# Performance work log

Measured on AMD Instinct MI355X. Metric: run time of the kernel, lower is better.

The kernel has to match this reference:

```python
import jax, jax.numpy as jnp
from jax import lax
import numpy as np

BETA = 0.9   # snn.Leaky(beta=0.9)
THR = 1.0    # snntorch default threshold, reset_mechanism='subtract'

@jax.custom_vjp
def spike(x):
    return (x > 0.0).astype(x.dtype)

def _spike_fwd(x):
    return spike(x), x

def _spike_bwd(x, g):
    # snntorch surrogate.atan (alpha=2): dS/dx = 1 / (1 + (pi*x)^2)
    return (g / (1.0 + (jnp.pi * x) ** 2),)

spike.defvjp(_spike_fwd, _spike_bwd)

def lif(inp, mem):
    # snntorch Leaky: reset based on PREVIOUS mem, detached; subtract mechanism
    reset = lax.stop_gradient(spike(mem - THR))
    mem = BETA * mem + inp - reset * THR
    return spike(mem - THR), mem

def conv1d(x, w, b):
    # x: (B, Cin, L), w: (Cout, Cin, K), VALID padding
    y = lax.conv_general_dilated(x, w, window_strides=(1,), padding='VALID',
                                 dimension_numbers=('NCH', 'OIH', 'NCH'))
    return y + b[None, :, None]

def setup_inputs() -> dict:
    key = jax.random.key(0)
    ks = jax.random.split(key, 11)
    B, L, T, num_c = 1024, 30, 100, 10
    def init(k, shape, fan_in):
        bound = 1.0 / np.sqrt(fan_in)
        return jax.random.uniform(k, shape, jnp.float32, -bound, bound)
    return {
        'x':   jax.random.normal(ks[0], (B, 1, L, T), jnp.float32),
        'w1':  init(ks[1], (16, 1, 7), 1 * 7),   'b1': init(ks[2], (16,), 7),
        'w2':  init(ks[3], (32, 16, 5), 16 * 5), 'b2': init(ks[4], (32,), 80),
        'w3':  init(ks[5], (64, 32, 3), 32 * 3), 'b3': init(ks[6], (64,), 96),
        'fw1': init(ks[7], (256, 64 * 18), 64 * 18), 'fb1': init(ks[8], (256,), 64 * 18),
        'fw2': init(ks[9], (num_c, 256), 256),       'fb2': init(ks[10], (num_c,), 256),
    }

def reference(x, w1, b1, w2, b2, w3, b3, fw1, fb1, fw2, fb2):
    B = x.shape[0]
    num_c = fw2.shape[0]
    xt_seq = jnp.transpose(x, (3, 0, 1, 2))  # (T, B, 1, 30)
    mems = (jnp.zeros((B, 16, 24), x.dtype),  # after conv1 (k=7): 30->24
            jnp.zeros((B, 32, 20), x.dtype),  # after conv2 (k=5): 24->20
            jnp.zeros((B, 64, 18), x.dtype),  # after conv3 (k=3): 20->18
            jnp.zeros((B, 256), x.dtype),
            jnp.zeros((B, num_c), x.dtype))
    def step(mems, xt):
        m1, m2, m3, m4, m5 = mems
        h = conv1d(xt, w1, b1); s, m1 = lif(h, m1)
        h = conv1d(s, w2, b2);  s, m2 = lif(h, m2)
        h = conv1d(s, w3, b3);  s, m3 = lif(h, m3)
        h = s.reshape(B, -1) @ fw1.T + fb1; s, m4 = lif(h, m4)
        h = s @ fw2.T + fb2;               s, m5 = lif(h, m5)
        return (m1, m2, m3, m4, m5), s
    _, spk_rec = lax.scan(step, mems, xt_seq)
    return spk_rec  # (T, B, num_c) -- matches torch.stack(spk_rec)
```

## Files before the change

kernel.cpp:

```cpp
#include <hip/hip_runtime.h>
#include <stdint.h>

#define BETA 0.9f

__global__ void transpose_fw1(const float* __restrict__ A, float* __restrict__ At) {
    __shared__ float tile[32][33];
    const int i0 = blockIdx.x * 32;
    const int j0 = blockIdx.y * 32;
    const int tx = threadIdx.x, ty = threadIdx.y;
    for (int r = ty; r < 32; r += 8)
        tile[r][tx] = A[(j0 + r) * 1152 + i0 + tx];
    __syncthreads();
    for (int r = ty; r < 32; r += 8)
        At[(i0 + r) * 256 + j0 + tx] = tile[tx][r];
}

__global__ __launch_bounds__(768)
__attribute__((amdgpu_waves_per_eu(6)))
void snn_main(
    const float* __restrict__ x,
    const float* __restrict__ w1, const float* __restrict__ b1,
    const float* __restrict__ w2, const float* __restrict__ b2,
    const float* __restrict__ w3, const float* __restrict__ b3,
    const float* __restrict__ fw1T,
    const float* __restrict__ fb1,
    const float* __restrict__ fw2, const float* __restrict__ fb2,
    float* __restrict__ out)
{
    const int b    = blockIdx.x;
    const int tid  = threadIdx.x;
    const int e    = (tid >= 384) ? 1 : 0;
    const int tl   = tid - 384 * e;
    const int lane = tid & 63;
    const int ew   = tl >> 6;

    __shared__ float w2L[16 * 5 * 32];
    __shared__ float w3L[32 * 3 * 64];
    __shared__ float pacc[2][6][256];
    __shared__ float s1e[2][16 * 24 + 8];
    __shared__ float s4[2][256];
    __shared__ unsigned long long masks[2][2][18];
    __shared__ unsigned int rm1[2][2][16];
    __shared__ unsigned int cm2[2][2][20];

    const int c1 = tl & 15;
    const int l1 = tl >> 4;
    const int c2 = tl & 31;
    const int g2 = tl >> 5;
    const int l02 = 2 * g2;
    const bool c2on = (ew < 5);
    const unsigned wmask2 = 0x3Fu << l02;
    const int c3 = lane;
    const int l03 = ew * 3;
    const int rl = tl - 320;

    for (int i = tid; i < 16 * 5 * 32; i += 768) {
        const int cc = i & 31, r = i >> 5;
        w2L[i] = w2[cc * 80 + r];
    }
    for (int i = tid; i < 32 * 3 * 64; i += 768) {
        const int cc = i & 63, r = i >> 6;
        w3L[i] = w3[cc * 96 + r];
    }
    if (tl < 16) { rm1[e][0][tl] = 0u; rm1[e][1][tl] = 0u; }
    if (tl < 20) { cm2[e][0][tl] = 0u; cm2[e][1][tl] = 0u; }
    if (tl < 8)  s1e[e][384 + tl] = 0.0f;

    float w1r[7];
#pragma unroll
    for (int k = 0; k < 7; ++k) w1r[k] = w1[c1 * 7 + k];
    const float b1r = b1[c1];
    const float b2r = b2[c2];
    const float b3r = b3[c3];
    const int jf = tl >> 4, chf = tl & 15;
    const float fb2r = (tl < 160 && chf == 0) ? fb2[jf] : 0.0f;
    float fb1q[4];
#pragma unroll
    for (int q = 0; q < 4; ++q)
        fb1q[q] = (ew == 5) ? fb1[rl + 64 * q] : 0.0f;

    float m1 = 0.f;
    float m2[2] = {0.f, 0.f};
    float m3[3] = {0.f, 0.f, 0.f};
    float m4q[4] = {0.f, 0.f, 0.f, 0.f};
    float m5 = 0.f;

    const float* xb = x + (2 * b + e) * 3000;
    const int out_b = (2 * b + e) * 10;
    const float4* fw1Tv = reinterpret_cast<const float4*>(fw1T);

    float xr[7];
#pragma unroll
    for (int k = 0; k < 7; ++k) xr[k] = xb[(l1 + k) * 100];

    __syncthreads();

    {
        float h = b1r;
#pragma unroll
        for (int k = 0; k < 7; ++k) h += xr[k] * w1r[k];
        float rs = (m1 > 1.0f) ? 1.0f : 0.0f;
        m1 = BETA * m1 + h - rs;
        float sa = (m1 > 1.0f) ? 1.0f : 0.0f;
        s1e[e][c1 * 24 + l1] = sa;
        if (sa != 0.0f) atomicOr(&rm1[e][0][c1], 1u << l1);
    }
    __syncthreads();

    for (int tau = 0; tau < 102; ++tau) {
        const int pb = tau & 1, pn = pb ^ 1;

        if (tl < 16) rm1[e][pn][tl] = 0u;
        if (tl < 20) cm2[e][pn][tl] = 0u;
        if (tau <= 98) {
#pragma unroll
            for (int k = 0; k < 7; ++k) xr[k] = xb[(l1 + k) * 100 + tau + 1];
        }
        if (c2on) {
            if (tau <= 99) {
                float h[2] = {b2r, b2r};
#pragma unroll
                for (int ci = 0; ci < 16; ++ci) {
                    const unsigned rmv =
                        __builtin_amdgcn_readfirstlane(rm1[e][pb][ci]);
                    if ((rmv & wmask2) == 0u) continue;
                    float win[6];
#pragma unroll
                    for (int r = 0; r < 6; ++r) win[r] = s1e[e][ci * 24 + l02 + r];
                    float wk[5];
#pragma unroll
                    for (int k = 0; k < 5; ++k) wk[k] = w2L[(ci * 5 + k) * 32 + c2];
#pragma unroll
                    for (int li = 0; li < 2; ++li)
#pragma unroll
                        for (int k = 0; k < 5; ++k) h[li] += win[li + k] * wk[k];
                }
#pragma unroll
                for (int li = 0; li < 2; ++li) {
                    float rs = (m2[li] > 1.0f) ? 1.0f : 0.0f;
                    m2[li] = BETA * m2[li] + h[li] - rs;
                    if (m2[li] > 1.0f) atomicOr(&cm2[e][pb][l02 + li], 1u << c2);
                }
            }
        } else {
            if (tau >= 2) {
#pragma unroll
                for (int q = 0; q < 4; ++q) {
                    const int j = rl + 64 * q;
                    float acc = fb1q[q];
#pragma unroll
                    for (int w = 0; w < 6; ++w) acc += pacc[e][w][j];
                    float rs = (m4q[q] > 1.0f) ? 1.0f : 0.0f;
                    m4q[q] = BETA * m4q[q] + acc - rs;
                    s4[e][j] = (m4q[q] > 1.0f) ? 1.0f : 0.0f;
                }
            }
        }
        __syncthreads();

        if (tau <= 98) {
            float h = b1r;
#pragma unroll
            for (int k = 0; k < 7; ++k) h += xr[k] * w1r[k];
            float rs = (m1 > 1.0f) ? 1.0f : 0.0f;
            m1 = BETA * m1 + h - rs;
            float sa = (m1 > 1.0f) ? 1.0f : 0.0f;
            s1e[e][c1 * 24 + l1] = sa;
            if (sa != 0.0f) atomicOr(&rm1[e][pn][c1], 1u << l1);
        }

        if (tau <= 99) {
            float h[3] = {b3r, b3r, b3r};
#pragma unroll
            for (int wl = 0; wl < 5; ++wl) {
                unsigned cm = __builtin_amdgcn_readfirstlane(cm2[e][pb][l03 + wl]);
                while (cm) {
                    const int ci = (int)__builtin_ctz(cm); cm &= cm - 1;
                    const float* wp = &w3L[ci * 192 + c3];
#pragma unroll
                    for (int k = 0; k < 3; ++k) {
                        const int li = wl - k;
                        if (li >= 0 && li < 3)
                            h[li] += wp[k * 64];
                    }
                }
            }
#pragma unroll
            for (int li = 0; li < 3; ++li) {
                float rs = (m3[li] > 1.0f) ? 1.0f : 0.0f;
                m3[li] = BETA * m3[li] + h[li] - rs;
                float s = (m3[li] > 1.0f) ? 1.0f : 0.0f;
                unsigned long long mk = __ballot(s != 0.0f);
                if (lane == 0) masks[e][pb][l03 + li] = mk;
            }
        }

        if (tau >= 1 && tau <= 100) {
            float4 acc4; acc4.x = acc4.y = acc4.z = acc4.w = 0.0f;
#pragma unroll 1
            for (int l = ew; l < 18; l += 6) {
                const unsigned* mp = (const unsigned*)&masks[e][pn][l];
                const unsigned mlo = __builtin_amdgcn_readfirstlane(mp[0]);
                const unsigned mhi = __builtin_amdgcn_readfirstlane(mp[1]);
                unsigned long long mk = ((unsigned long long)mhi << 32) | mlo;
                while (mk) {
                    float4 f0, f1, f2, f3;
                    f0.x=f0.y=f0.z=f0.w=0.f; f1=f0; f2=f0; f3=f0;
                    int c;
                    c = (int)__builtin_ctzll(mk); mk &= mk - 1;
                    f0 = fw1Tv[(c * 18 + l) * 64 + lane];
                    if (mk) { c = (int)__builtin_ctzll(mk); mk &= mk - 1;
                              f1 = fw1Tv[(c * 18 + l) * 64 + lane]; }
                    if (mk) { c = (int)__builtin_ctzll(mk); mk &= mk - 1;
                              f2 = fw1Tv[(c * 18 + l) * 64 + lane]; }
                    if (mk) { c = (int)__builtin_ctzll(mk); mk &= mk - 1;
                              f3 = fw1Tv[(c * 18 + l) * 64 + lane]; }
                    acc4.x += f0.x; acc4.y += f0.y; acc4.z += f0.z; acc4.w += f0.w;
                    acc4.x += f1.x; acc4.y += f1.y; acc4.z += f1.z; acc4.w += f1.w;
                    acc4.x += f2.x; acc4.y += f2.y; acc4.z += f2.z; acc4.w += f2.w;
                    acc4.x += f3.x; acc4.y += f3.y; acc4.z += f3.z; acc4.w += f3.w;
                }
            }
            ((float4*)&pacc[e][ew][0])[lane] = acc4;
        }

        if (tau >= 2 && tl < 160) {
            const int t5 = tau - 2;
            const float* wrow = fw2 + jf * 256;
            float p = 0.f;
#pragma unroll
            for (int i = 0; i < 16; ++i)
                p += s4[e][i * 16 + chf] * wrow[i * 16 + chf];
            p += __shfl_xor(p, 8, 16);
            p += __shfl_xor(p, 4, 16);
            p += __shfl_xor(p, 2, 16);
            p += __shfl_xor(p, 1, 16);
            if (chf == 0) {
                float h = fb2r + p;
                float rs = (m5 > 1.0f) ? 1.0f : 0.0f;
                m5 = BETA * m5 + h - rs;
                out[t5 * 10240 + out_b + jf] = (m5 > 1.0f) ? 1.0f : 0.0f;
            }
        }
        __syncthreads();
    }
}

extern "C" void kernel_launch(void* const* d_in, const int* in_sizes, int n_in,
                              void* d_out, int out_size, void* d_ws, size_t ws_size,
                              hipStream_t stream) {
    const float* x   = (const float*)d_in[0];
    const float* w1  = (const float*)d_in[1];
    const float* b1  = (const float*)d_in[2];
    const float* w2  = (const float*)d_in[3];
    const float* b2  = (const float*)d_in[4];
    const float* w3  = (const float*)d_in[5];
    const float* b3  = (const float*)d_in[6];
    const float* fw1 = (const float*)d_in[7];
    const float* fb1 = (const float*)d_in[8];
    const float* fw2 = (const float*)d_in[9];
    const float* fb2 = (const float*)d_in[10];
    float* out  = (float*)d_out;
    float* fw1T = (float*)d_ws;

    dim3 tb(32, 8);
    dim3 tg(1152 / 32, 256 / 32);
    transpose_fw1<<<tg, tb, 0, stream>>>(fw1, fw1T);
    snn_main<<<512, 768, 0, stream>>>(x, w1, b1, w2, b2, w3, b3,
                                      fw1T, fb1, fw2, fb2, out);
}
```

Baseline: 679.5 us.

## Restage SNN pipeline to cut one step of latency and use bitmask conv2

Reorders the per-timestep phases so conv3 and the output layer run in one barrier interval and conv1 plus fc1 run in the next. This shortens the pipeline from 102 to 101 iterations and lets the masks buffer be single-buffered. Conv2 now reads spike bits directly from the bitmask and does conditional adds instead of multiply-adds over a shared spike array, so s1e is removed. The w3 shared layout is changed to [ci][c][k], which adds strided-by-3 LDS access per lane and so risks bank conflicts.

After: 677.9 us. Within noise of the previous version (-0.2%).

```diff
diff --git a/kernel.cpp b/kernel.cpp
--- a/kernel.cpp
+++ b/kernel.cpp
@@ -35,11 +35,10 @@
     const int ew   = tl >> 6;
 
     __shared__ float w2L[16 * 5 * 32];
-    __shared__ float w3L[32 * 3 * 64];
+    __shared__ float w3L[32 * 64 * 3];
     __shared__ float pacc[2][6][256];
-    __shared__ float s1e[2][16 * 24 + 8];
     __shared__ float s4[2][256];
-    __shared__ unsigned long long masks[2][2][18];
+    __shared__ unsigned long long masks[2][18];
     __shared__ unsigned int rm1[2][2][16];
     __shared__ unsigned int cm2[2][2][20];
 
@@ -48,8 +47,7 @@
     const int c2 = tl & 31;
     const int g2 = tl >> 5;
     const int l02 = 2 * g2;
-    const bool c2on = (ew < 5);
-    const unsigned wmask2 = 0x3Fu << l02;
+    const bool c2w = (ew < 5);
     const int c3 = lane;
     const int l03 = ew * 3;
     const int rl = tl - 320;
@@ -58,13 +56,13 @@
         const int cc = i & 31, r = i >> 5;
         w2L[i] = w2[cc * 80 + r];
     }
-    for (int i = tid; i < 32 * 3 * 64; i += 768) {
-        const int cc = i & 63, r = i >> 6;
-        w3L[i] = w3[cc * 96 + r];
+    for (int i = tid; i < 32 * 64 * 3; i += 768) {
+        const int ci = i / 192, r2 = i - ci * 192;
+        const int cc = r2 / 3, k = r2 - cc * 3;
+        w3L[i] = w3[cc * 96 + ci * 3 + k];
     }
     if (tl < 16) { rm1[e][0][tl] = 0u; rm1[e][1][tl] = 0u; }
     if (tl < 20) { cm2[e][0][tl] = 0u; cm2[e][1][tl] = 0u; }
-    if (tl < 8)  s1e[e][384 + tl] = 0.0f;
 
     float w1r[7];
 #pragma unroll
@@ -101,13 +99,11 @@
         for (int k = 0; k < 7; ++k) h += xr[k] * w1r[k];
         float rs = (m1 > 1.0f) ? 1.0f : 0.0f;
         m1 = BETA * m1 + h - rs;
-        float sa = (m1 > 1.0f) ? 1.0f : 0.0f;
-        s1e[e][c1 * 24 + l1] = sa;
-        if (sa != 0.0f) atomicOr(&rm1[e][0][c1], 1u << l1);
+        if (m1 > 1.0f) atomicOr(&rm1[e][0][c1], 1u << l1);
     }
     __syncthreads();
 
-    for (int tau = 0; tau < 102; ++tau) {
+    for (int tau = 0; tau <= 100; ++tau) {
         const int pb = tau & 1, pn = pb ^ 1;
 
         if (tl < 16) rm1[e][pn][tl] = 0u;
@@ -116,58 +112,48 @@
 #pragma unroll
             for (int k = 0; k < 7; ++k) xr[k] = xb[(l1 + k) * 100 + tau + 1];
         }
-        if (c2on) {
+        if (c2w) {
             if (tau <= 99) {
-                float h[2] = {b2r, b2r};
+                float h0 = b2r, h1 = b2r;
 #pragma unroll
                 for (int ci = 0; ci < 16; ++ci) {
                     const unsigned rmv =
                         __builtin_amdgcn_readfirstlane(rm1[e][pb][ci]);
-                    if ((rmv & wmask2) == 0u) continue;
-                    float win[6];
-#pragma unroll
-                    for (int r = 0; r < 6; ++r) win[r] = s1e[e][ci * 24 + l02 + r];
+                    const unsigned wb = (rmv >> l02) & 0x3Fu;
+                    if (wb == 0u) continue;
                     float wk[5];
 #pragma unroll
-                    for (int k = 0; k < 5; ++k) wk[k] = w2L[(ci * 5 + k) * 32 + c2];
-#pragma unroll
-                    for (int li = 0; li < 2; ++li)
-#pragma unroll
-                        for (int k = 0; k < 5; ++k) h[li] += win[li + k] * wk[k];
-                }
-#pragma unroll
-                for (int li = 0; li < 2; ++li) {
-                    float rs = (m2[li] > 1.0f) ? 1.0f : 0.0f;
-                    m2[li] = BETA * m2[li] + h[li] - rs;
-                    if (m2[li] > 1.0f) atomicOr(&cm2[e][pb][l02 + li], 1u << c2);
-                }
-            }
-        } else {
-            if (tau >= 2) {
-#pragma unroll
-                for (int q = 0; q < 4; ++q) {
-                    const int j = rl + 64 * q;
-                    float acc = fb1q[q];
-#pragma unroll
-                    for (int w = 0; w < 6; ++w) acc += pacc[e][w][j];
-                    float rs = (m4q[q] > 1.0f) ? 1.0f : 0.0f;
-                    m4q[q] = BETA * m4q[q] + acc - rs;
-                    s4[e][j] = (m4q[q] > 1.0f) ? 1.0f : 0.0f;
-                }
+                    for (int k = 0; k < 5; ++k)
+                        wk[k] = w2L[(ci * 5 + k) * 32 + c2];
+                    if (wb & 1u)  h0 += wk[0];
+                    if (wb & 2u)  { h0 += wk[1]; h1 += wk[0]; }
+                    if (wb & 4u)  { h0 += wk[2]; h1 += wk[1]; }
+                    if (wb & 8u)  { h0 += wk[3]; h1 += wk[2]; }
+                    if (wb & 16u) { h0 += wk[4]; h1 += wk[3]; }
+                    if (wb & 32u) h1 += wk[4];
+                }
+                {
+                    float rs = (m2[0] > 1.0f) ? 1.0f : 0.0f;
+                    m2[0] = BETA * m2[0] + h0 - rs;
+                    if (m2[0] > 1.0f) atomicOr(&cm2[e][pb][l02], 1u << c2);
+                    rs = (m2[1] > 1.0f) ? 1.0f : 0.0f;
+                    m2[1] = BETA * m2[1] + h1 - rs;
+                    if (m2[1] > 1.0f) atomicOr(&cm2[e][pb][l02 + 1], 1u << c2);
+                }
+            }
+        } else if (tau >= 1) {
+#pragma unroll
+            for (int q = 0; q < 4; ++q) {
+                const int j = rl + 64 * q;
+                float acc = fb1q[q];
+#pragma unroll
+                for (int w = 0; w < 6; ++w) acc += pacc[e][w][j];
+                float rs = (m4q[q] > 1.0f) ? 1.0f : 0.0f;
+                m4q[q] = BETA * m4q[q] + acc - rs;
+                s4[e][j] = (m4q[q] > 1.0f) ? 1.0f : 0.0f;
             }
         }
         __syncthreads();
-
-        if (tau <= 98) {
-            float h = b1r;
-#pragma unroll
-            for (int k = 0; k < 7; ++k) h += xr[k] * w1r[k];
-            float rs = (m1 > 1.0f) ? 1.0f : 0.0f;
-            m1 = BETA * m1 + h - rs;
-            float sa = (m1 > 1.0f) ? 1.0f : 0.0f;
-            s1e[e][c1 * 24 + l1] = sa;
-            if (sa != 0.0f) atomicOr(&rm1[e][pn][c1], 1u << l1);
-        }
 
         if (tau <= 99) {
             float h[3] = {b3r, b3r, b3r};
@@ -176,12 +162,12 @@
                 unsigned cm = __builtin_amdgcn_readfirstlane(cm2[e][pb][l03 + wl]);
                 while (cm) {
                     const int ci = (int)__builtin_ctz(cm); cm &= cm - 1;
-                    const float* wp = &w3L[ci * 192 + c3];
+                    const float* wp = &w3L[ci * 192 + c3 * 3];
 #pragma unroll
                     for (int k = 0; k < 3; ++k) {
                         const int li = wl - k;
                         if (li >= 0 && li < 3)
-                            h[li] += wp[k * 64];
+                            h[li] += wp[k];
                     }
                 }
             }
@@ -191,15 +177,43 @@
                 m3[li] = BETA * m3[li] + h[li] - rs;
                 float s = (m3[li] > 1.0f) ? 1.0f : 0.0f;
                 unsigned long long mk = __ballot(s != 0.0f);
-                if (lane == 0) masks[e][pb][l03 + li] = mk;
-            }
-        }
-
-        if (tau >= 1 && tau <= 100) {
+                if (lane == 0) masks[e][l03 + li] = mk;
+            }
+        }
+        if (tau >= 1 && tl < 160) {
+            const int t5 = tau - 1;
+            const float* wrow = fw2 + jf * 256;
+            float p = 0.f;
+#pragma unroll
+            for (int i = 0; i < 16; ++i)
+                p += s4[e][i * 16 + chf] * wrow[i * 16 + chf];
+            p += __shfl_xor(p, 8, 16);
+            p += __shfl_xor(p, 4, 16);
+            p += __shfl_xor(p, 2, 16);
+            p += __shfl_xor(p, 1, 16);
+            if (chf == 0) {
+                float h = fb2r + p;
+                float rs = (m5 > 1.0f) ? 1.0f : 0.0f;
+                m5 = BETA * m5 + h - rs;
+                out[t5 * 10240 + out_b + jf] = (m5 > 1.0f) ? 1.0f : 0.0f;
+            }
+        }
+        __syncthreads();
+
+        if (tau <= 98) {
+            float h = b1r;
+#pragma unroll
+            for (int k = 0; k < 7; ++k) h += xr[k] * w1r[k];
+            float rs = (m1 > 1.0f) ? 1.0f : 0.0f;
+            m1 = BETA * m1 + h - rs;
+            if (m1 > 1.0f) atomicOr(&rm1[e][pn][c1], 1u << l1);
+        }
+
+        if (tau <= 99) {
             float4 acc4; acc4.x = acc4.y = acc4.z = acc4.w = 0.0f;
 #pragma unroll 1
             for (int l = ew; l < 18; l += 6) {
-                const unsigned* mp = (const unsigned*)&masks[e][pn][l];
+                const unsigned* mp = (const unsigned*)&masks[e][l];
                 const unsigned mlo = __builtin_amdgcn_readfirstlane(mp[0]);
                 const unsigned mhi = __builtin_amdgcn_readfirstlane(mp[1]);
                 unsigned long long mk = ((unsigned long long)mhi << 32) | mlo;
@@ -223,25 +237,6 @@
             }
             ((float4*)&pacc[e][ew][0])[lane] = acc4;
         }
-
-        if (tau >= 2 && tl < 160) {
-            const int t5 = tau - 2;
-            const float* wrow = fw2 + jf * 256;
-            float p = 0.f;
-#pragma unroll
-            for (int i = 0; i < 16; ++i)
-                p += s4[e][i * 16 + chf] * wrow[i * 16 + chf];
-            p += __shfl_xor(p, 8, 16);
-            p += __shfl_xor(p, 4, 16);
-            p += __shfl_xor(p, 2, 16);
-            p += __shfl_xor(p, 1, 16);
-            if (chf == 0) {
-                float h = fb2r + p;
-                float rs = (m5 > 1.0f) ? 1.0f : 0.0f;
-                m5 = BETA * m5 + h - rs;
-                out[t5 * 10240 + out_b + jf] = (m5 > 1.0f) ? 1.0f : 0.0f;
-            }
-        }
         __syncthreads();
     }
 }
```

## Restructure timestep pipeline: fuse FC2 into FC1 wave, add barrier phase

Applied to the files above, without the earlier changes.

Moves the layer-5 (fc2 + LIF) computation into the sixth wave, right after the fc1 LIF update, so s4 is consumed in the same phase it is produced. Conv3 gets its own barrier-separated phase, which removes one stage of pipeline delay: the loop runs 101 iterations instead of 102 and the masks buffer is no longer double-buffered. The cost is a third __syncthreads per timestep and fc2 work serialized onto a single wave, with each lane group handling up to three outputs.

Measured after the change: 779.6 us. 1.15x slower.

```diff
diff --git a/kernel.cpp b/kernel.cpp
--- a/kernel.cpp
+++ b/kernel.cpp
@@ -39,7 +39,7 @@
     __shared__ float pacc[2][6][256];
     __shared__ float s1e[2][16 * 24 + 8];
     __shared__ float s4[2][256];
-    __shared__ unsigned long long masks[2][2][18];
+    __shared__ unsigned long long masks[2][18];
     __shared__ unsigned int rm1[2][2][16];
     __shared__ unsigned int cm2[2][2][20];
 
@@ -48,11 +48,11 @@
     const int c2 = tl & 31;
     const int g2 = tl >> 5;
     const int l02 = 2 * g2;
-    const bool c2on = (ew < 5);
+    const bool c2w = (ew < 5);
     const unsigned wmask2 = 0x3Fu << l02;
     const int c3 = lane;
     const int l03 = ew * 3;
-    const int rl = tl - 320;
+    const int g5 = lane >> 4, chf5 = lane & 15;
 
     for (int i = tid; i < 16 * 5 * 32; i += 768) {
         const int cc = i & 31, r = i >> 5;
@@ -72,18 +72,21 @@
     const float b1r = b1[c1];
     const float b2r = b2[c2];
     const float b3r = b3[c3];
-    const int jf = tl >> 4, chf = tl & 15;
-    const float fb2r = (tl < 160 && chf == 0) ? fb2[jf] : 0.0f;
-    float fb1q[4];
+    float fb1q[4], fb2q[3];
 #pragma unroll
     for (int q = 0; q < 4; ++q)
-        fb1q[q] = (ew == 5) ? fb1[rl + 64 * q] : 0.0f;
+        fb1q[q] = (ew == 5) ? fb1[lane + 64 * q] : 0.0f;
+#pragma unroll
+    for (int pi = 0; pi < 3; ++pi) {
+        const int jj = g5 + 4 * pi;
+        fb2q[pi] = (ew == 5 && chf5 == 0 && jj < 10) ? fb2[jj] : 0.0f;
+    }
 
     float m1 = 0.f;
     float m2[2] = {0.f, 0.f};
     float m3[3] = {0.f, 0.f, 0.f};
     float m4q[4] = {0.f, 0.f, 0.f, 0.f};
-    float m5 = 0.f;
+    float m5q[3] = {0.f, 0.f, 0.f};
 
     const float* xb = x + (2 * b + e) * 3000;
     const int out_b = (2 * b + e) * 10;
@@ -107,7 +110,7 @@
     }
     __syncthreads();
 
-    for (int tau = 0; tau < 102; ++tau) {
+    for (int tau = 0; tau <= 100; ++tau) {
         const int pb = tau & 1, pn = pb ^ 1;
 
         if (tl < 16) rm1[e][pn][tl] = 0u;
@@ -116,7 +119,7 @@
 #pragma unroll
             for (int k = 0; k < 7; ++k) xr[k] = xb[(l1 + k) * 100 + tau + 1];
         }
-        if (c2on) {
+        if (c2w) {
             if (tau <= 99) {
                 float h[2] = {b2r, b2r};
 #pragma unroll
@@ -142,18 +145,66 @@
                     if (m2[li] > 1.0f) atomicOr(&cm2[e][pb][l02 + li], 1u << c2);
                 }
             }
-        } else {
-            if (tau >= 2) {
-#pragma unroll
-                for (int q = 0; q < 4; ++q) {
-                    const int j = rl + 64 * q;
-                    float acc = fb1q[q];
-#pragma unroll
-                    for (int w = 0; w < 6; ++w) acc += pacc[e][w][j];
-                    float rs = (m4q[q] > 1.0f) ? 1.0f : 0.0f;
-                    m4q[q] = BETA * m4q[q] + acc - rs;
-                    s4[e][j] = (m4q[q] > 1.0f) ? 1.0f : 0.0f;
-                }
+        } else if (tau >= 1) {
+            const int t45 = tau - 1;
+#pragma unroll
+            for (int q = 0; q < 4; ++q) {
+                const int j = lane + 64 * q;
+                float acc = fb1q[q];
+#pragma unroll
+                for (int w = 0; w < 6; ++w) acc += pacc[e][w][j];
+                float rs = (m4q[q] > 1.0f) ? 1.0f : 0.0f;
+                m4q[q] = BETA * m4q[q] + acc - rs;
+                s4[e][j] = (m4q[q] > 1.0f) ? 1.0f : 0.0f;
+            }
+#pragma unroll
+            for (int pi = 0; pi < 3; ++pi) {
+                const int jj = g5 + 4 * pi;
+                if (jj < 10) {
+                    const float* wrow = fw2 + jj * 256;
+                    float p = 0.f;
+#pragma unroll
+                    for (int i = 0; i < 16; ++i)
+                        p += s4[e][i * 16 + chf5] * wrow[i * 16 + chf5];
+                    p += __shfl_xor(p, 8, 16);
+                    p += __shfl_xor(p, 4, 16);
+                    p += __shfl_xor(p, 2, 16);
+                    p += __shfl_xor(p, 1, 16);
+                    if (chf5 == 0) {
+                        float h = fb2q[pi] + p;
+                        float rs = (m5q[pi] > 1.0f) ? 1.0f : 0.0f;
+                        m5q[pi] = BETA * m5q[pi] + h - rs;
+                        out[t45 * 10240 + out_b + jj] =
+                            (m5q[pi] > 1.0f) ? 1.0f : 0.0f;
+                    }
+                }
+            }
+        }
+        __syncthreads();
+
+        if (tau <= 99) {
+            float h[3] = {b3r, b3r, b3r};
+#pragma unroll
+            for (int wl = 0; wl < 5; ++wl) {
+                unsigned cm = __builtin_amdgcn_readfirstlane(cm2[e][pb][l03 + wl]);
+                while (cm) {
+                    const int ci = (int)__builtin_ctz(cm); cm &= cm - 1;
+                    const float* wp = &w3L[ci * 192 + c3];
+#pragma unroll
+                    for (int k = 0; k < 3; ++k) {
+                        const int li = wl - k;
+                        if (li >= 0 && li < 3)
+                            h[li] += wp[k * 64];
+                    }
+                }
+            }
+#pragma unroll
+            for (int li = 0; li < 3; ++li) {
+                float rs = (m3[li] > 1.0f) ? 1.0f : 0.0f;
+                m3[li] = BETA * m3[li] + h[li] - rs;
+                float s = (m3[li] > 1.0f) ? 1.0f : 0.0f;
+                unsigned long long mk = __ballot(s != 0.0f);
+                if (lane == 0) masks[e][l03 + li] = mk;
             }
         }
         __syncthreads();
@@ -170,36 +221,10 @@
         }
 
         if (tau <= 99) {
-            float h[3] = {b3r, b3r, b3r};
-#pragma unroll
-            for (int wl = 0; wl < 5; ++wl) {
-                unsigned cm = __builtin_amdgcn_readfirstlane(cm2[e][pb][l03 + wl]);
-                while (cm) {
-                    const int ci = (int)__builtin_ctz(cm); cm &= cm - 1;
-                    const float* wp = &w3L[ci * 192 + c3];
-#pragma unroll
-                    for (int k = 0; k < 3; ++k) {
-                        const int li = wl - k;
-                        if (li >= 0 && li < 3)
-                            h[li] += wp[k * 64];
-                    }
-                }
-            }
-#pragma unroll
-            for (int li = 0; li < 3; ++li) {
-                float rs = (m3[li] > 1.0f) ? 1.0f : 0.0f;
-                m3[li] = BETA * m3[li] + h[li] - rs;
-                float s = (m3[li] > 1.0f) ? 1.0f : 0.0f;
-                unsigned long long mk = __ballot(s != 0.0f);
-                if (lane == 0) masks[e][pb][l03 + li] = mk;
-            }
-        }
-
-        if (tau >= 1 && tau <= 100) {
             float4 acc4; acc4.x = acc4.y = acc4.z = acc4.w = 0.0f;
 #pragma unroll 1
             for (int l = ew; l < 18; l += 6) {
-                const unsigned* mp = (const unsigned*)&masks[e][pn][l];
+                const unsigned* mp = (const unsigned*)&masks[e][l];
                 const unsigned mlo = __builtin_amdgcn_readfirstlane(mp[0]);
                 const unsigned mhi = __builtin_amdgcn_readfirstlane(mp[1]);
                 unsigned long long mk = ((unsigned long long)mhi << 32) | mlo;
@@ -223,25 +248,6 @@
             }
             ((float4*)&pacc[e][ew][0])[lane] = acc4;
         }
-
-        if (tau >= 2 && tl < 160) {
-            const int t5 = tau - 2;
-            const float* wrow = fw2 + jf * 256;
-            float p = 0.f;
-#pragma unroll
-            for (int i = 0; i < 16; ++i)
-                p += s4[e][i * 16 + chf] * wrow[i * 16 + chf];
-            p += __shfl_xor(p, 8, 16);
-            p += __shfl_xor(p, 4, 16);
-            p += __shfl_xor(p, 2, 16);
-            p += __shfl_xor(p, 1, 16);
-            if (chf == 0) {
-                float h = fb2r + p;
-                float rs = (m5 > 1.0f) ? 1.0f : 0.0f;
-                m5 = BETA * m5 + h - rs;
-                out[t5 * 10240 + out_b + jf] = (m5 > 1.0f) ? 1.0f : 0.0f;
-            }
-        }
         __syncthreads();
     }
 }
```
